# Performance work log

Hardware: AMD Instinct MI355X
Metric: run time of the kernel (lower is better)

Reference implementation:

```python
import jax, jax.numpy as jnp
import numpy as np

B, T, I, H, NCLS = 256, 784, 1, 110, 10


def setup_inputs() -> dict:
    key = jax.random.key(0)
    ks = jax.random.split(key, 10)
    s = 1.0 / np.sqrt(H)
    u = lambda k, shape: jax.random.uniform(k, shape, jnp.float32, -s, s)
    return {
        "x": jax.random.normal(ks[0], (B, T, I), jnp.float32),
        "W_ih": u(ks[1], (4 * H, I)),
        "W_hh": u(ks[2], (4 * H, H)),
        "b": u(ks[3], (4 * H,)),
        "W_p": u(ks[4], (1, H)),     # skip-gate readout of cell state
        "b_p": jnp.ones((1,), jnp.float32),  # bias init ~1 -> start by updating
        "h0": u(ks[5], (H,)),        # learned initial hidden (learn_init=True)
        "c0": u(ks[6], (H,)),        # learned initial cell
        "W_fc": u(ks[7], (NCLS, H)),
        "b_fc": u(ks[8], (NCLS,)),
    }


def _st_round(u):
    # straight-through binarization: round in fwd, identity grad in bwd
    return u + jax.lax.stop_gradient(jnp.round(u) - u)


def reference(x, W_ih, W_hh, b, W_p, b_p, h0, c0, W_fc, b_fc):
    Bsz = x.shape[0]
    Hh = h0.shape[0]
    xT = jnp.transpose(x, (1, 0, 2))  # [T, B, I] (the permute in Net.forward)
    h = jnp.broadcast_to(h0, (Bsz, Hh))
    c = jnp.broadcast_to(c0, (Bsz, Hh))
    u0 = jnp.ones((Bsz, 1), x.dtype)  # first step always updates

    def step(carry, xt):
        h, c, u = carry
        ub = _st_round(u)                                  # binary update gate [B,1]
        gates = xt @ W_ih.T + h @ W_hh.T + b               # [B, 4H]
        i, f, g, o = jnp.split(gates, 4, axis=-1)
        i = jax.nn.sigmoid(i)
        f = jax.nn.sigmoid(f)
        o = jax.nn.sigmoid(o)
        g = jnp.tanh(g)
        c_new = f * c + i * g
        h_new = o * jnp.tanh(c_new)
        c_n = ub * c_new + (1.0 - ub) * c                  # skip: keep old state
        h_n = ub * h_new + (1.0 - ub) * h
        du = jax.nn.sigmoid(c_n @ W_p.T + b_p)             # delta-u from cell [B,1]
        u_n = ub * du + (1.0 - ub) * (u + jnp.minimum(du, 1.0 - u))
        return (h_n, c_n, u_n), (h_n, ub)

    (h_last, _, _), (hs, ubs) = jax.lax.scan(step, (h, c, u0), xT)
    out = hs[-1] @ W_fc.T + b_fc                           # fc on last timestep
    total_u = jnp.sum(ubs)                                 # total number of updates
    return out, total_u[None]
```

## Files before the change

### kernel.cpp

```cpp
#include <hip/hip_runtime.h>
#include <stdint.h>


#define T784 784
#define H110 110
#define NT   256
#define NCLS 10
#define LOG2E 1.44269504088896340736f
#define WQS  (0.09535f / 127.0f)

__device__ __forceinline__ float frcp(float x)  { return __builtin_amdgcn_rcpf(x); }
__device__ __forceinline__ float fexp2(float x) { return __builtin_amdgcn_exp2f(x); }

__device__ __forceinline__ float add_q1(float v) {
    float d; asm("v_add_f32_dpp %0, %1, %1 quad_perm:[1,0,3,2] row_mask:0xf bank_mask:0xf bound_ctrl:0"
                 : "=v"(d) : "v"(v)); return d;
}
__device__ __forceinline__ float add_q2(float v) {
    float d; asm("v_add_f32_dpp %0, %1, %1 quad_perm:[2,3,0,1] row_mask:0xf bank_mask:0xf bound_ctrl:0"
                 : "=v"(d) : "v"(v)); return d;
}
__device__ __forceinline__ float add_hm(float v) {
    float d; asm("v_add_f32_dpp %0, %1, %1 row_half_mirror row_mask:0xf bank_mask:0xf bound_ctrl:0"
                 : "=v"(d) : "v"(v)); return d;
}
__device__ __forceinline__ float add_rm(float v) {
    float d; asm("v_add_f32_dpp %0, %1, %1 row_mirror row_mask:0xf bank_mask:0xf bound_ctrl:0"
                 : "=v"(d) : "v"(v)); return d;
}
__device__ __forceinline__ float add_b15(float v) {
    float d; asm("v_add_f32_dpp %0, %1, %1 row_bcast:15 row_mask:0xf bank_mask:0xf bound_ctrl:0"
                 : "=v"(d) : "v"(v)); return d;
}
__device__ __forceinline__ float add_b31(float v) {
    float d; asm("v_add_f32_dpp %0, %1, %1 row_bcast:31 row_mask:0xf bank_mask:0xf bound_ctrl:0"
                 : "=v"(d) : "v"(v)); return d;
}
template <int L>
__device__ __forceinline__ float qbcast(float v) {
    float d;
    if (L == 0) asm("v_mov_b32_dpp %0, %1 quad_perm:[0,0,0,0] row_mask:0xf bank_mask:0xf bound_ctrl:0" : "=v"(d) : "v"(v));
    if (L == 1) asm("v_mov_b32_dpp %0, %1 quad_perm:[1,1,1,1] row_mask:0xf bank_mask:0xf bound_ctrl:0" : "=v"(d) : "v"(v));
    if (L == 2) asm("v_mov_b32_dpp %0, %1 quad_perm:[2,2,2,2] row_mask:0xf bank_mask:0xf bound_ctrl:0" : "=v"(d) : "v"(v));
    if (L == 3) asm("v_mov_b32_dpp %0, %1 quad_perm:[3,3,3,3] row_mask:0xf bank_mask:0xf bound_ctrl:0" : "=v"(d) : "v"(v));
    return d;
}

__device__ __forceinline__ int qpack(float f0, float f1, float f2, float f3) {
    const int q0 = (int)rintf(f0) & 0xFF;
    const int q1 = (int)rintf(f1) & 0xFF;
    const int q2 = (int)rintf(f2) & 0xFF;
    const int q3 = (int)rintf(f3) & 0xFF;
    return q0 | (q1 << 8) | (q2 << 16) | (q3 << 24);
}

__global__ __launch_bounds__(NT, 1)
void skiplstm_kernel(const float* __restrict__ x,
                     const float* __restrict__ W_ih,
                     const float* __restrict__ W_hh,
                     const float* __restrict__ b,
                     const float* __restrict__ W_p,
                     const float* __restrict__ b_p,
                     const float* __restrict__ h0,
                     const float* __restrict__ c0,
                     const float* __restrict__ W_fc,
                     const float* __restrict__ b_fc,
                     float* __restrict__ out)
{
    __shared__ int   s_h8[2][32];
    __shared__ float s_pbuf[256];
    __shared__ float s_x[T784];

    const int tid  = threadIdx.x;
    const int bb   = blockIdx.x;
    const int q    = tid >> 2;
    const int j    = tid & 3;
    const int uA   = 2 * q;
    const int uB   = 2 * q + 1;
    const bool qact = (q < 55);

    const float qinv = 1.0f / WQS;
    int wA[4][7], wB[4][7];
    float bvA[4], wvA[4], bvB[4], wvB[4];
    #pragma unroll
    for (int g = 0; g < 4; ++g) {
        const float gfac = (g == 2) ? (-2.0f * LOG2E) : (-LOG2E);
        const int rowA = uA + H110 * g;
        const int rowB = uB + H110 * g;
        bvA[g] = (qact && j == 0) ? b[rowA]    * gfac : 0.0f;
        wvA[g] = (qact && j == 0) ? W_ih[rowA] * gfac : 0.0f;
        bvB[g] = (qact && j == 0) ? b[rowB]    * gfac : 0.0f;
        wvB[g] = (qact && j == 0) ? W_ih[rowB] * gfac : 0.0f;
        const float* rpA = W_hh + rowA * H110;
        const float* rpB = W_hh + rowB * H110;
        #pragma unroll
        for (int d = 0; d < 7; ++d) {
            float fa[4], fb[4];
            #pragma unroll
            for (int e = 0; e < 4; ++e) {
                const int k = 28 * j + 4 * d + e;
                fa[e] = (qact && k < H110) ? rpA[k] * qinv : 0.0f;
                fb[e] = (qact && k < H110) ? rpB[k] * qinv : 0.0f;
            }
            wA[g][d] = qpack(fa[0], fa[1], fa[2], fa[3]);
            wB[g][d] = qpack(fb[0], fb[1], fb[2], fb[3]);
        }
    }
    const float scg[4] = { (WQS / 127.0f) * (-LOG2E), (WQS / 127.0f) * (-LOG2E),
                           (WQS / 127.0f) * (-2.0f * LOG2E), (WQS / 127.0f) * (-LOG2E) };

    float cregA = qact ? c0[uA] : 0.0f;
    float hregA = qact ? h0[uA] : 0.0f;
    float cregB = qact ? c0[uB] : 0.0f;
    float hregB = qact ? h0[uB] : 0.0f;
    const float wpnA = qact ? (-LOG2E) * W_p[uA] : 0.0f;
    const float wpnB = qact ? (-LOG2E) * W_p[uB] : 0.0f;
    const float bpn  = (-LOG2E) * b_p[0];

    const float mulc = (j == 2) ? 2.0f : 1.0f;
    const float addc = (j == 2) ? -1.0f : 0.0f;

    for (int i = tid; i < 64;   i += NT) ((int*)s_h8)[i] = 0;
    for (int i = tid; i < 256;  i += NT) s_pbuf[i] = 0.0f;
    for (int i = tid; i < T784; i += NT) s_x[i] = x[bb * T784 + i];
    __syncthreads();
    if (tid < H110)
        ((int8_t*)s_h8[0])[tid] = (int8_t)__float2int_rn(h0[tid] * 127.0f);
    __syncthreads();

    float u_prev = 1.0f;
    int   cnt    = 0;

    auto step = [&](const int* hb, int* hn,
                    const float* pp, float* pn, int t, bool first) {
        const int lane = tid & 63;
        const float p0 = pp[lane], p1 = pp[lane + 64];
        const float xt = s_x[t];
        int hd[7];
        #pragma unroll
        for (int d = 0; d < 7; ++d) hd[d] = hb[7 * j + d];

        int ia0 = 0, ia1 = 0, ia2 = 0, ia3 = 0;
        int ib0 = 0, ib1 = 0, ib2 = 0, ib3 = 0;
        #pragma unroll
        for (int d = 0; d < 7; ++d) {
            ia0 = __builtin_amdgcn_sdot4(hd[d], wA[0][d], ia0, false);
            ia1 = __builtin_amdgcn_sdot4(hd[d], wA[1][d], ia1, false);
            ia2 = __builtin_amdgcn_sdot4(hd[d], wA[2][d], ia2, false);
            ia3 = __builtin_amdgcn_sdot4(hd[d], wA[3][d], ia3, false);
            ib0 = __builtin_amdgcn_sdot4(hd[d], wB[0][d], ib0, false);
            ib1 = __builtin_amdgcn_sdot4(hd[d], wB[1][d], ib1, false);
            ib2 = __builtin_amdgcn_sdot4(hd[d], wB[2][d], ib2, false);
            ib3 = __builtin_amdgcn_sdot4(hd[d], wB[3][d], ib3, false);
        }
        float a0 = fmaf((float)ia0, scg[0], fmaf(xt, wvA[0], bvA[0]));
        float a1 = fmaf((float)ia1, scg[1], fmaf(xt, wvA[1], bvA[1]));
        float a2 = fmaf((float)ia2, scg[2], fmaf(xt, wvA[2], bvA[2]));
        float a3 = fmaf((float)ia3, scg[3], fmaf(xt, wvA[3], bvA[3]));
        float b0 = fmaf((float)ib0, scg[0], fmaf(xt, wvB[0], bvB[0]));
        float b1 = fmaf((float)ib1, scg[1], fmaf(xt, wvB[1], bvB[1]));
        float b2 = fmaf((float)ib2, scg[2], fmaf(xt, wvB[2], bvB[2]));
        float b3 = fmaf((float)ib3, scg[3], fmaf(xt, wvB[3], bvB[3]));

        float u_now;
        if (first) {
            u_now = 1.0f;
        } else {
            float v = p0 + p1;
            v = add_q1(v); v = add_q2(v); v = add_hm(v);
            v = add_rm(v); v = add_b15(v); v = add_b31(v);
            const float tot = __int_as_float(
                __builtin_amdgcn_readlane(__float_as_int(v), 63));
            const float du = frcp(1.0f + fexp2(tot + bpn));
            u_now = (u_prev > 0.5f) ? du
                                    : (u_prev + fminf(du, 1.0f - u_prev));
        }
        const bool up = u_now > 0.5f;
        cnt += up ? 1 : 0;
        u_prev = u_now;

        a0 = add_q1(a0); a1 = add_q1(a1); a2 = add_q1(a2); a3 = add_q1(a3);
        b0 = add_q1(b0); b1 = add_q1(b1); b2 = add_q1(b2); b3 = add_q1(b3);
        a0 = add_q2(a0); a1 = add_q2(a1); a2 = add_q2(a2); a3 = add_q2(a3);
        b0 = add_q2(b0); b1 = add_q2(b1); b2 = add_q2(b2); b3 = add_q2(b3);

        const float tA01  = (j & 1) ? a1 : a0;
        const float tA23  = (j & 1) ? a3 : a2;
        const float aselA = (j & 2) ? tA23 : tA01;
        const float tB01  = (j & 1) ? b1 : b0;
        const float tB23  = (j & 1) ? b3 : b2;
        const float aselB = (j & 2) ? tB23 : tB01;
        const float avA = fmaf(mulc, frcp(1.0f + fexp2(aselA)), addc);
        const float avB = fmaf(mulc, frcp(1.0f + fexp2(aselB)), addc);
        const float giA = qbcast<0>(avA);
        const float gfA = qbcast<1>(avA);
        const float ggA = qbcast<2>(avA);
        const float goA = qbcast<3>(avA);
        const float giB = qbcast<0>(avB);
        const float gfB = qbcast<1>(avB);
        const float ggB = qbcast<2>(avB);
        const float goB = qbcast<3>(avB);

        const float cnA = fmaf(gfA, cregA, giA * ggA);
        const float cnB = fmaf(gfB, cregB, giB * ggB);
        const float thA = fmaf(2.0f, frcp(1.0f + fexp2(cnA * (-2.0f * LOG2E))), -1.0f);
        const float thB = fmaf(2.0f, frcp(1.0f + fexp2(cnB * (-2.0f * LOG2E))), -1.0f);
        const float hnA = goA * thA;
        const float hnB = goB * thB;
        cregA = up ? cnA : cregA;
        hregA = up ? hnA : hregA;
        cregB = up ? cnB : cregB;
        hregB = up ? hnB : hregB;
        if (qact && j == 0) {
            ((int8_t*)hn)[uA] = (int8_t)__float2int_rn(hregA * 127.0f);
            pn[uA] = cregA * wpnA;
        }
        if (qact && j == 1) {
            ((int8_t*)hn)[uB] = (int8_t)__float2int_rn(hregB * 127.0f);
            pn[uB] = cregB * wpnB;
        }
        __syncthreads();
    };

    int* const h0b = s_h8[0];
    int* const h1b = s_h8[1];
    float* const p0b = s_pbuf;
    float* const p1b = s_pbuf + 128;

    step(h0b, h1b, p0b, p1b, 0, true);
    step(h1b, h0b, p1b, p0b, 1, false);
    step(h0b, h1b, p0b, p1b, 2, false);
    step(h1b, h0b, p1b, p0b, 3, false);
    for (int t = 4; t < T784; t += 4) {
        step(h0b, h1b, p0b, p1b, t,     false);
        step(h1b, h0b, p1b, p0b, t + 1, false);
        step(h0b, h1b, p0b, p1b, t + 2, false);
        step(h1b, h0b, p1b, p0b, t + 3, false);
    }

    if (qact && j == 0) s_pbuf[uA] = hregA;
    if (qact && j == 1) s_pbuf[uB] = hregB;
    __syncthreads();
    if (tid < NCLS) {
        float acc = b_fc[tid];
        for (int k = 0; k < H110; ++k)
            acc = fmaf(s_pbuf[k], W_fc[tid * H110 + k], acc);
        out[bb * NCLS + tid] = acc;
    }
    if (tid == 0)
        atomicAdd(out + 256 * NCLS, (float)cnt);
}

__global__ void zero_tail_kernel(float* out) {
    if (threadIdx.x == 0) out[256 * NCLS] = 0.0f;
}

extern "C" void kernel_launch(void* const* d_in, const int* in_sizes, int n_in,
                              void* d_out, int out_size, void* d_ws, size_t ws_size,
                              hipStream_t stream) {
    const float* x    = (const float*)d_in[0];
    const float* W_ih = (const float*)d_in[1];
    const float* W_hh = (const float*)d_in[2];
    const float* b    = (const float*)d_in[3];
    const float* W_p  = (const float*)d_in[4];
    const float* b_p  = (const float*)d_in[5];
    const float* h0   = (const float*)d_in[6];
    const float* c0   = (const float*)d_in[7];
    const float* W_fc = (const float*)d_in[8];
    const float* b_fc = (const float*)d_in[9];
    float* out = (float*)d_out;

    zero_tail_kernel<<<1, 64, 0, stream>>>(out);
    skiplstm_kernel<<<256, NT, 0, stream>>>(x, W_ih, W_hh, b, W_p, b_p,
                                            h0, c0, W_fc, b_fc, out);
}
```

Before: 507.1 us.

## Remap work so each thread owns one full gate row across 512 threads

Doubles the block to 512 threads and gives each thread one whole gate row (unit q, gate j) with all 28 packed int8 weight words, replacing the old scheme where a quad of lanes split the K dimension across two units. This removes the per-step cross-lane DPP reductions and the gate-select logic, at the cost of more sdot4 work per thread, a full h-vector LDS read per thread, and more waves taking part in every per-step barrier. The kernel's existing buffers and host launch code are left unchanged, so whether the 512-thread mapping still lines up with the 256-entry p buffer and the launch configuration depends on code not shown. Launch bounds change to allow two blocks per CU.

```diff
diff --git a/kernel.cpp b/kernel.cpp
--- a/kernel.cpp
+++ b/kernel.cpp
@@ -4,7 +4,7 @@
 
 #define T784 784
 #define H110 110
-#define NT   256
+#define NT   512
 #define NCLS 10
 #define LOG2E 1.44269504088896340736f
 #define WQS  (0.09535f / 127.0f)
@@ -54,7 +54,7 @@
     return q0 | (q1 << 8) | (q2 << 16) | (q3 << 24);
 }
 
-__global__ __launch_bounds__(NT, 1)
+__global__ __launch_bounds__(NT, 2)
 void skiplstm_kernel(const float* __restrict__ x,
                      const float* __restrict__ W_ih,
                      const float* __restrict__ W_hh,
@@ -75,47 +75,33 @@
     const int bb   = blockIdx.x;
     const int q    = tid >> 2;
     const int j    = tid & 3;
-    const int uA   = 2 * q;
-    const int uB   = 2 * q + 1;
-    const bool qact = (q < 55);
+    const bool qact = (q < H110);
 
     const float qinv = 1.0f / WQS;
-    int wA[4][7], wB[4][7];
-    float bvA[4], wvA[4], bvB[4], wvB[4];
-    #pragma unroll
-    for (int g = 0; g < 4; ++g) {
-        const float gfac = (g == 2) ? (-2.0f * LOG2E) : (-LOG2E);
-        const int rowA = uA + H110 * g;
-        const int rowB = uB + H110 * g;
-        bvA[g] = (qact && j == 0) ? b[rowA]    * gfac : 0.0f;
-        wvA[g] = (qact && j == 0) ? W_ih[rowA] * gfac : 0.0f;
-        bvB[g] = (qact && j == 0) ? b[rowB]    * gfac : 0.0f;
-        wvB[g] = (qact && j == 0) ? W_ih[rowB] * gfac : 0.0f;
-        const float* rpA = W_hh + rowA * H110;
-        const float* rpB = W_hh + rowB * H110;
+    const float gfac = (j == 2) ? (-2.0f * LOG2E) : (-LOG2E);
+    const int   row  = j * H110 + q;
+    const float bv = qact ? b[row]    * gfac : 0.0f;
+    const float wv = qact ? W_ih[row] * gfac : 0.0f;
+    const float scj = (WQS / 127.0f) * gfac;
+    int w[28];
+    {
+        const float* rp = W_hh + row * H110;
         #pragma unroll
-        for (int d = 0; d < 7; ++d) {
-            float fa[4], fb[4];
+        for (int d = 0; d < 28; ++d) {
+            float f[4];
             #pragma unroll
             for (int e = 0; e < 4; ++e) {
-                const int k = 28 * j + 4 * d + e;
-                fa[e] = (qact && k < H110) ? rpA[k] * qinv : 0.0f;
-                fb[e] = (qact && k < H110) ? rpB[k] * qinv : 0.0f;
+                const int k = 4 * d + e;
+                f[e] = (qact && k < H110) ? rp[k] * qinv : 0.0f;
             }
-            wA[g][d] = qpack(fa[0], fa[1], fa[2], fa[3]);
-            wB[g][d] = qpack(fb[0], fb[1], fb[2], fb[3]);
+            w[d] = qpack(f[0], f[1], f[2], f[3]);
         }
     }
-    const float scg[4] = { (WQS / 127.0f) * (-LOG2E), (WQS / 127.0f) * (-LOG2E),
-                           (WQS / 127.0f) * (-2.0f * LOG2E), (WQS / 127.0f) * (-LOG2E) };
-
-    float cregA = qact ? c0[uA] : 0.0f;
-    float hregA = qact ? h0[uA] : 0.0f;
-    float cregB = qact ? c0[uB] : 0.0f;
-    float hregB = qact ? h0[uB] : 0.0f;
-    const float wpnA = qact ? (-LOG2E) * W_p[uA] : 0.0f;
-    const float wpnB = qact ? (-LOG2E) * W_p[uB] : 0.0f;
-    const float bpn  = (-LOG2E) * b_p[0];
+
+    float creg = qact ? c0[q] : 0.0f;
+    float hreg = qact ? h0[q] : 0.0f;
+    const float wpn = qact ? (-LOG2E) * W_p[q] : 0.0f;
+    const float bpn = (-LOG2E) * b_p[0];
 
     const float mulc = (j == 2) ? 2.0f : 1.0f;
     const float addc = (j == 2) ? -1.0f : 0.0f;
@@ -136,31 +122,24 @@
         const int lane = tid & 63;
         const float p0 = pp[lane], p1 = pp[lane + 64];
         const float xt = s_x[t];
-        int hd[7];
-        #pragma unroll
-        for (int d = 0; d < 7; ++d) hd[d] = hb[7 * j + d];
-
-        int ia0 = 0, ia1 = 0, ia2 = 0, ia3 = 0;
-        int ib0 = 0, ib1 = 0, ib2 = 0, ib3 = 0;
+        int h8[28];
         #pragma unroll
         for (int d = 0; d < 7; ++d) {
-            ia0 = __builtin_amdgcn_sdot4(hd[d], wA[0][d], ia0, false);
-            ia1 = __builtin_amdgcn_sdot4(hd[d], wA[1][d], ia1, false);
-            ia2 = __builtin_amdgcn_sdot4(hd[d], wA[2][d], ia2, false);
-            ia3 = __builtin_amdgcn_sdot4(hd[d], wA[3][d], ia3, false);
-            ib0 = __builtin_amdgcn_sdot4(hd[d], wB[0][d], ib0, false);
-            ib1 = __builtin_amdgcn_sdot4(hd[d], wB[1][d], ib1, false);
-            ib2 = __builtin_amdgcn_sdot4(hd[d], wB[2][d], ib2, false);
-            ib3 = __builtin_amdgcn_sdot4(hd[d], wB[3][d], ib3, false);
-        }
-        float a0 = fmaf((float)ia0, scg[0], fmaf(xt, wvA[0], bvA[0]));
-        float a1 = fmaf((float)ia1, scg[1], fmaf(xt, wvA[1], bvA[1]));
-        float a2 = fmaf((float)ia2, scg[2], fmaf(xt, wvA[2], bvA[2]));
-        float a3 = fmaf((float)ia3, scg[3], fmaf(xt, wvA[3], bvA[3]));
-        float b0 = fmaf((float)ib0, scg[0], fmaf(xt, wvB[0], bvB[0]));
-        float b1 = fmaf((float)ib1, scg[1], fmaf(xt, wvB[1], bvB[1]));
-        float b2 = fmaf((float)ib2, scg[2], fmaf(xt, wvB[2], bvB[2]));
-        float b3 = fmaf((float)ib3, scg[3], fmaf(xt, wvB[3], bvB[3]));
+            const int4 v = ((const int4*)hb)[d];
+            h8[4 * d + 0] = v.x; h8[4 * d + 1] = v.y;
+            h8[4 * d + 2] = v.z; h8[4 * d + 3] = v.w;
+        }
+
+        int ia0 = 0, ia1 = 0, ia2 = 0, ia3 = 0;
+        #pragma unroll
+        for (int d = 0; d < 7; ++d) {
+            ia0 = __builtin_amdgcn_sdot4(h8[4 * d + 0], w[4 * d + 0], ia0, false);
+            ia1 = __builtin_amdgcn_sdot4(h8[4 * d + 1], w[4 * d + 1], ia1, false);
+            ia2 = __builtin_amdgcn_sdot4(h8[4 * d + 2], w[4 * d + 2], ia2, false);
+            ia3 = __builtin_amdgcn_sdot4(h8[4 * d + 3], w[4 * d + 3], ia3, false);
+        }
+        const int ia = (ia0 + ia1) + (ia2 + ia3);
+        const float asel = fmaf((float)ia, scj, fmaf(xt, wv, bv));
 
         float u_now;
         if (first) {
@@ -179,45 +158,20 @@
         cnt += up ? 1 : 0;
         u_prev = u_now;
 
-        a0 = add_q1(a0); a1 = add_q1(a1); a2 = add_q1(a2); a3 = add_q1(a3);
-        b0 = add_q1(b0); b1 = add_q1(b1); b2 = add_q1(b2); b3 = add_q1(b3);
-        a0 = add_q2(a0); a1 = add_q2(a1); a2 = add_q2(a2); a3 = add_q2(a3);
-        b0 = add_q2(b0); b1 = add_q2(b1); b2 = add_q2(b2); b3 = add_q2(b3);
-
-        const float tA01  = (j & 1) ? a1 : a0;
-        const float tA23  = (j & 1) ? a3 : a2;
-        const float aselA = (j & 2) ? tA23 : tA01;
-        const float tB01  = (j & 1) ? b1 : b0;
-        const float tB23  = (j & 1) ? b3 : b2;
-        const float aselB = (j & 2) ? tB23 : tB01;
-        const float avA = fmaf(mulc, frcp(1.0f + fexp2(aselA)), addc);
-        const float avB = fmaf(mulc, frcp(1.0f + fexp2(aselB)), addc);
-        const float giA = qbcast<0>(avA);
-        const float gfA = qbcast<1>(avA);
-        const float ggA = qbcast<2>(avA);
-        const float goA = qbcast<3>(avA);
-        const float giB = qbcast<0>(avB);
-        const float gfB = qbcast<1>(avB);
-        const float ggB = qbcast<2>(avB);
-        const float goB = qbcast<3>(avB);
-
-        const float cnA = fmaf(gfA, cregA, giA * ggA);
-        const float cnB = fmaf(gfB, cregB, giB * ggB);
-        const float thA = fmaf(2.0f, frcp(1.0f + fexp2(cnA * (-2.0f * LOG2E))), -1.0f);
-        const float thB = fmaf(2.0f, frcp(1.0f + fexp2(cnB * (-2.0f * LOG2E))), -1.0f);
-        const float hnA = goA * thA;
-        const float hnB = goB * thB;
-        cregA = up ? cnA : cregA;
-        hregA = up ? hnA : hregA;
-        cregB = up ? cnB : cregB;
-        hregB = up ? hnB : hregB;
+        const float av = fmaf(mulc, frcp(1.0f + fexp2(asel)), addc);
+        const float gi = qbcast<0>(av);
+        const float gf = qbcast<1>(av);
+        const float gg = qbcast<2>(av);
+        const float go = qbcast<3>(av);
+
+        const float cn = fmaf(gf, creg, gi * gg);
+        const float th = fmaf(2.0f, frcp(1.0f + fexp2(cn * (-2.0f * LOG2E))), -1.0f);
+        const float hn_ = go * th;
+        creg = up ? cn : creg;
+        hreg = up ? hn_ : hreg;
         if (qact && j == 0) {
-            ((int8_t*)hn)[uA] = (int8_t)__float2int_rn(hregA * 127.0f);
-            pn[uA] = cregA * wpnA;
-        }
-        if (qact && j == 1) {
-            ((int8_t*)hn)[uB] = (int8_t)__float2int_rn(hregB * 127.0f);
-            pn[uB] = cregB * wpnB;
+            ((int8_t*)hn)[q] = (int8_t)__float2int_rn(hreg * 127.0f);
+            pn[q] = creg * wpn;
         }
         __syncthreads();
     };
@@ -238,8 +192,7 @@
         step(h1b, h0b, p1b, p0b, t + 3, false);
     }
 
-    if (qact && j == 0) s_pbuf[uA] = hregA;
-    if (qact && j == 1) s_pbuf[uB] = hregB;
+    if (qact && j == 0) s_pbuf[q] = hreg;
     __syncthreads();
     if (tid < NCLS) {
         float acc = b_fc[tid];
```

After: 467.0 us. 1.09x faster.
